# Kernel tuning notes

Measured on AMD Instinct MI355X. Metric: run time of the kernel, lower is better.

The kernel has to match this reference:

```python
import jax, jax.numpy as jnp
import numpy as np

B, IN_F, OUT_F, FAN_IN = 2048, 4096, 4096, 32


def setup_inputs() -> dict:
    key = jax.random.key(0)
    k1, k2, k3, k4 = jax.random.split(key, 4)
    x = jax.random.normal(k1, (B, IN_F), dtype=jnp.float32)
    weight = jax.random.normal(k2, (OUT_F, FAN_IN), dtype=jnp.float32) * (1.0 / np.sqrt(FAN_IN))
    bias = jax.random.normal(k3, (OUT_F,), dtype=jnp.float32) * 0.01
    indx_seqs = jnp.sort(jax.random.randint(k4, (OUT_F, FAN_IN), 0, IN_F, dtype=jnp.int64), axis=1)
    return {"x": x, "weight": weight, "bias": bias, "indx_seqs": indx_seqs}


def reference(x, weight, bias, indx_seqs):
    # gather: (B, OUT_F, FAN_IN) -- input[:, indx_seqs]
    gathered = jnp.take(x, indx_seqs, axis=1)
    # elementwise multiply by weight (OUT_F, FAN_IN), reduce over fan_in, add bias
    return jnp.sum(weight * gathered, axis=2) + bias
```

## Files before the change

kernel.cpp:

```cpp
#include <hip/hip_runtime.h>


constexpr int IN_F  = 4096;
constexpr int OUT_F = 4096;
constexpr int K     = 32;
constexpr int BT    = 8;
constexpr int THREADS = 512;
constexpr int ROWS_PER_BLOCK = 32;
constexpr int ITERS = ROWS_PER_BLOCK / BT;
constexpr int CPT = IN_F / THREADS;

typedef __fp16 h2_t __attribute__((ext_vector_type(2)));

__device__ __forceinline__ int pack_f16(float lo, float hi) {
    union { h2_t h; int i; } cv;
    cv.h = __builtin_amdgcn_cvt_pkrtz(lo, hi);
    return cv.i;
}
__device__ __forceinline__ float h_lo(int u) {
    union { int i; h2_t h; } cv; cv.i = u; return (float)cv.h[0];
}
__device__ __forceinline__ float h_hi(int u) {
    union { int i; h2_t h; } cv; cv.i = u; return (float)cv.h[1];
}

__global__ __launch_bounds__(THREADS)
void lc_kernel(const float* __restrict__ x,
               const float* __restrict__ w,
               const float* __restrict__ bias,
               const int* __restrict__ idx,
               float* __restrict__ out,
               int bchunks) {
    __shared__ int4 xs[IN_F];
    const int tid = threadIdx.x;
    const int ochunk = blockIdx.x / bchunks;
    const int bchunk = blockIdx.x % bchunks;
    const int o = ochunk * THREADS + tid;

    int   ao[K];
    float wr[K];
    const int4*   ip = reinterpret_cast<const int4*>(idx + (size_t)o * K);
    const float4* wp = reinterpret_cast<const float4*>(w + (size_t)o * K);
#pragma unroll
    for (int kk = 0; kk < K / 4; ++kk) {
        int4   i4 = ip[kk];
        float4 w4 = wp[kk];
        ao[4*kk+0] = i4.x << 4;  ao[4*kk+1] = i4.y << 4;
        ao[4*kk+2] = i4.z << 4;  ao[4*kk+3] = i4.w << 4;
        wr[4*kk+0] = w4.x;  wr[4*kk+1] = w4.y;
        wr[4*kk+2] = w4.z;  wr[4*kk+3] = w4.w;
    }
    const float bv = bias[o];
    const int b0 = bchunk * ROWS_PER_BLOCK;

    float pf[BT * CPT];

    {
        const float* xr = x + (size_t)b0 * IN_F;
#pragma unroll
        for (int j = 0; j < CPT; ++j)
#pragma unroll
            for (int r = 0; r < BT; ++r)
                pf[j * BT + r] = xr[(size_t)r * IN_F + tid + j * THREADS];
#pragma unroll
        for (int j = 0; j < CPT; ++j) {
            int4 pk;
            pk.x = pack_f16(pf[j*BT+0], pf[j*BT+1]);
            pk.y = pack_f16(pf[j*BT+2], pf[j*BT+3]);
            pk.z = pack_f16(pf[j*BT+4], pf[j*BT+5]);
            pk.w = pack_f16(pf[j*BT+6], pf[j*BT+7]);
            xs[tid + j * THREADS] = pk;
        }
    }
    __syncthreads();

    const char* xb = reinterpret_cast<const char*>(&xs[0]);

#pragma unroll
    for (int it = 0; it < ITERS; ++it) {
        if (it + 1 < ITERS) {
            const float* xr = x + (size_t)(b0 + (it + 1) * BT) * IN_F;
#pragma unroll
            for (int j = 0; j < CPT; ++j)
#pragma unroll
                for (int r = 0; r < BT; ++r)
                    pf[j * BT + r] = xr[(size_t)r * IN_F + tid + j * THREADS];
        }

        float acc[BT];
#pragma unroll
        for (int r = 0; r < BT; ++r) acc[r] = bv;
#pragma unroll
        for (int k = 0; k < K; ++k) {
            int4 v = *reinterpret_cast<const int4*>(xb + ao[k]);
            const float wk = wr[k];
            acc[0] += wk * h_lo(v.x);
            acc[1] += wk * h_hi(v.x);
            acc[2] += wk * h_lo(v.y);
            acc[3] += wk * h_hi(v.y);
            acc[4] += wk * h_lo(v.z);
            acc[5] += wk * h_hi(v.z);
            acc[6] += wk * h_lo(v.w);
            acc[7] += wk * h_hi(v.w);
        }

        float* op = out + (size_t)(b0 + it * BT) * OUT_F + o;
#pragma unroll
        for (int r = 0; r < BT; ++r) op[(size_t)r * OUT_F] = acc[r];

        if (it + 1 < ITERS) {
            __syncthreads();
#pragma unroll
            for (int j = 0; j < CPT; ++j) {
                int4 pk;
                pk.x = pack_f16(pf[j*BT+0], pf[j*BT+1]);
                pk.y = pack_f16(pf[j*BT+2], pf[j*BT+3]);
                pk.z = pack_f16(pf[j*BT+4], pf[j*BT+5]);
                pk.w = pack_f16(pf[j*BT+6], pf[j*BT+7]);
                xs[tid + j * THREADS] = pk;
            }
            __syncthreads();
        }
    }
}

extern "C" void kernel_launch(void* const* d_in, const int* in_sizes, int n_in,
                              void* d_out, int out_size, void* d_ws, size_t ws_size,
                              hipStream_t stream) {
    const float* x    = (const float*)d_in[0];
    const float* w    = (const float*)d_in[1];
    const float* bias = (const float*)d_in[2];
    const int*   idx  = (const int*)d_in[3];
    float* out = (float*)d_out;

    const int Bv = in_sizes[0] / IN_F;
    const int bchunks = Bv / ROWS_PER_BLOCK;
    const int ochunks = (in_sizes[1] / K) / THREADS;
    lc_kernel<<<dim3(ochunks * bchunks), dim3(THREADS), 0, stream>>>(
        x, w, bias, idx, out, bchunks);
}
```

Baseline: 41.30 us.

## Pre-pack x to fp16 in workspace and DMA tiles into LDS via global_load_lds

Adds a prep kernel that converts x into an fp16 interleaved layout (8 batch rows per 16-byte entry) in the workspace. The main kernel then loads each 64KB tile straight into LDS with global_load_lds and computes one 8-row group per block of 256 threads. This removes the per-block fp32 load, convert and LDS store path and the multi-iteration sync loop. The cost is an extra kernel launch, an extra write and read of the packed x buffer, and many more blocks that each reload idx and weights. The original kernel is kept as a fallback when the workspace is too small.

After: 67.60 us. 63.7% more time.

```diff
diff --git a/kernel.cpp b/kernel.cpp
--- a/kernel.cpp
+++ b/kernel.cpp
@@ -5,10 +5,8 @@
 constexpr int OUT_F = 4096;
 constexpr int K     = 32;
 constexpr int BT    = 8;
-constexpr int THREADS = 512;
-constexpr int ROWS_PER_BLOCK = 32;
-constexpr int ITERS = ROWS_PER_BLOCK / BT;
-constexpr int CPT = IN_F / THREADS;
+constexpr int MT    = 256;
+constexpr long long XT_BYTES = (long long)(2048 / BT) * IN_F * 16;
 
 typedef __fp16 h2_t __attribute__((ext_vector_type(2)));
 
@@ -24,18 +22,110 @@
     union { int i; h2_t h; } cv; cv.i = u; return (float)cv.h[1];
 }
 
-__global__ __launch_bounds__(THREADS)
-void lc_kernel(const float* __restrict__ x,
-               const float* __restrict__ w,
-               const float* __restrict__ bias,
-               const int* __restrict__ idx,
-               float* __restrict__ out,
-               int bchunks) {
+__global__ __launch_bounds__(256)
+void lc_prep(const float* __restrict__ x, int4* __restrict__ xT) {
+    const int bid  = blockIdx.x;
+    const int g    = bid >> 2;
+    const int part = bid & 3;
+    const int q    = part * 256 + threadIdx.x;
+    const float4* xr = reinterpret_cast<const float4*>(x + (size_t)g * BT * IN_F);
+    float4 r[BT];
+#pragma unroll
+    for (int i = 0; i < BT; ++i) r[i] = xr[(size_t)i * (IN_F / 4) + q];
+    int4* op = xT + (size_t)g * IN_F + 4 * q;
+#pragma unroll
+    for (int m = 0; m < 4; ++m) {
+        int4 pk;
+        pk.x = pack_f16(((const float*)&r[0])[m], ((const float*)&r[1])[m]);
+        pk.y = pack_f16(((const float*)&r[2])[m], ((const float*)&r[3])[m]);
+        pk.z = pack_f16(((const float*)&r[4])[m], ((const float*)&r[5])[m]);
+        pk.w = pack_f16(((const float*)&r[6])[m], ((const float*)&r[7])[m]);
+        op[m] = pk;
+    }
+}
+
+__global__ __launch_bounds__(MT)
+void lc_main(const int4* __restrict__ xT,
+             const float* __restrict__ w,
+             const float* __restrict__ bias,
+             const int* __restrict__ idx,
+             float* __restrict__ out,
+             int groups) {
+    __shared__ int4 xs[IN_F];
+    const int tid = threadIdx.x;
+    const int g   = blockIdx.x % groups;
+    const int oc  = blockIdx.x / groups;
+    const int o   = oc * MT + tid;
+
+    int   ao[K];
+    float wr[K];
+    const int4*   ip = reinterpret_cast<const int4*>(idx + (size_t)o * K);
+    const float4* wp = reinterpret_cast<const float4*>(w + (size_t)o * K);
+    int4   iq[K / 4];
+    float4 wq[K / 4];
+#pragma unroll
+    for (int kk = 0; kk < K / 4; ++kk) { iq[kk] = ip[kk]; wq[kk] = wp[kk]; }
+    const float bv = bias[o];
+
+    {
+        const char* gsrc = reinterpret_cast<const char*>(xT) + (size_t)g * (IN_F * 16);
+        char* lbase = reinterpret_cast<char*>(&xs[0]);
+        const int wbase = (tid & 192) << 4;
+        const int lane16 = tid << 4;
+#pragma unroll
+        for (int j = 0; j < 16; ++j) {
+            __builtin_amdgcn_global_load_lds(
+                (const __attribute__((address_space(1))) unsigned int*)(gsrc + j * 4096 + lane16),
+                (__attribute__((address_space(3))) unsigned int*)(lbase + j * 4096 + wbase),
+                16, 0, 0);
+        }
+    }
+    __syncthreads();
+
+#pragma unroll
+    for (int kk = 0; kk < K / 4; ++kk) {
+        ao[4*kk+0] = iq[kk].x << 4;  ao[4*kk+1] = iq[kk].y << 4;
+        ao[4*kk+2] = iq[kk].z << 4;  ao[4*kk+3] = iq[kk].w << 4;
+        wr[4*kk+0] = wq[kk].x;  wr[4*kk+1] = wq[kk].y;
+        wr[4*kk+2] = wq[kk].z;  wr[4*kk+3] = wq[kk].w;
+    }
+
+    const char* xb = reinterpret_cast<const char*>(&xs[0]);
+    float acc[BT];
+#pragma unroll
+    for (int r = 0; r < BT; ++r) acc[r] = bv;
+#pragma unroll
+    for (int k = 0; k < K; ++k) {
+        int4 v = *reinterpret_cast<const int4*>(xb + ao[k]);
+        const float wk = wr[k];
+        acc[0] += wk * h_lo(v.x);  acc[1] += wk * h_hi(v.x);
+        acc[2] += wk * h_lo(v.y);  acc[3] += wk * h_hi(v.y);
+        acc[4] += wk * h_lo(v.z);  acc[5] += wk * h_hi(v.z);
+        acc[6] += wk * h_lo(v.w);  acc[7] += wk * h_hi(v.w);
+    }
+
+    float* op = out + (size_t)(g * BT) * OUT_F + o;
+#pragma unroll
+    for (int r = 0; r < BT; ++r) op[(size_t)r * OUT_F] = acc[r];
+}
+
+constexpr int FB_THREADS = 512;
+constexpr int FB_RPB = 32;
+constexpr int FB_ITERS = FB_RPB / BT;
+constexpr int FB_CPT = IN_F / FB_THREADS;
+
+__global__ __launch_bounds__(FB_THREADS)
+void lc_fallback(const float* __restrict__ x,
+                 const float* __restrict__ w,
+                 const float* __restrict__ bias,
+                 const int* __restrict__ idx,
+                 float* __restrict__ out,
+                 int bchunks) {
     __shared__ int4 xs[IN_F];
     const int tid = threadIdx.x;
     const int ochunk = blockIdx.x / bchunks;
     const int bchunk = blockIdx.x % bchunks;
-    const int o = ochunk * THREADS + tid;
+    const int o = ochunk * FB_THREADS + tid;
 
     int   ao[K];
     float wr[K];
@@ -51,42 +141,39 @@
         wr[4*kk+2] = w4.z;  wr[4*kk+3] = w4.w;
     }
     const float bv = bias[o];
-    const int b0 = bchunk * ROWS_PER_BLOCK;
-
-    float pf[BT * CPT];
+    const int b0 = bchunk * FB_RPB;
+    float pf[BT * FB_CPT];
 
     {
         const float* xr = x + (size_t)b0 * IN_F;
 #pragma unroll
-        for (int j = 0; j < CPT; ++j)
+        for (int j = 0; j < FB_CPT; ++j)
 #pragma unroll
             for (int r = 0; r < BT; ++r)
-                pf[j * BT + r] = xr[(size_t)r * IN_F + tid + j * THREADS];
-#pragma unroll
-        for (int j = 0; j < CPT; ++j) {
+                pf[j * BT + r] = xr[(size_t)r * IN_F + tid + j * FB_THREADS];
+#pragma unroll
+        for (int j = 0; j < FB_CPT; ++j) {
             int4 pk;
             pk.x = pack_f16(pf[j*BT+0], pf[j*BT+1]);
             pk.y = pack_f16(pf[j*BT+2], pf[j*BT+3]);
             pk.z = pack_f16(pf[j*BT+4], pf[j*BT+5]);
             pk.w = pack_f16(pf[j*BT+6], pf[j*BT+7]);
-            xs[tid + j * THREADS] = pk;
+            xs[tid + j * FB_THREADS] = pk;
         }
     }
     __syncthreads();
-
     const char* xb = reinterpret_cast<const char*>(&xs[0]);
 
 #pragma unroll
-    for (int it = 0; it < ITERS; ++it) {
-        if (it + 1 < ITERS) {
+    for (int it = 0; it < FB_ITERS; ++it) {
+        if (it + 1 < FB_ITERS) {
             const float* xr = x + (size_t)(b0 + (it + 1) * BT) * IN_F;
 #pragma unroll
-            for (int j = 0; j < CPT; ++j)
+            for (int j = 0; j < FB_CPT; ++j)
 #pragma unroll
                 for (int r = 0; r < BT; ++r)
-                    pf[j * BT + r] = xr[(size_t)r * IN_F + tid + j * THREADS];
-        }
-
+                    pf[j * BT + r] = xr[(size_t)r * IN_F + tid + j * FB_THREADS];
+        }
         float acc[BT];
 #pragma unroll
         for (int r = 0; r < BT; ++r) acc[r] = bv;
@@ -94,30 +181,25 @@
         for (int k = 0; k < K; ++k) {
             int4 v = *reinterpret_cast<const int4*>(xb + ao[k]);
             const float wk = wr[k];
-            acc[0] += wk * h_lo(v.x);
-            acc[1] += wk * h_hi(v.x);
-            acc[2] += wk * h_lo(v.y);
-            acc[3] += wk * h_hi(v.y);
-            acc[4] += wk * h_lo(v.z);
-            acc[5] += wk * h_hi(v.z);
-            acc[6] += wk * h_lo(v.w);
-            acc[7] += wk * h_hi(v.w);
-        }
-
+            acc[0] += wk * h_lo(v.x);  acc[1] += wk * h_hi(v.x);
+            acc[2] += wk * h_lo(v.y);  acc[3] += wk * h_hi(v.y);
+            acc[4] += wk * h_lo(v.z);  acc[5] += wk * h_hi(v.z);
+            acc[6] += wk * h_lo(v.w);  acc[7] += wk * h_hi(v.w);
+        }
         float* op = out + (size_t)(b0 + it * BT) * OUT_F + o;
 #pragma unroll
         for (int r = 0; r < BT; ++r) op[(size_t)r * OUT_F] = acc[r];
 
-        if (it + 1 < ITERS) {
+        if (it + 1 < FB_ITERS) {
             __syncthreads();
 #pragma unroll
-            for (int j = 0; j < CPT; ++j) {
+            for (int j = 0; j < FB_CPT; ++j) {
                 int4 pk;
                 pk.x = pack_f16(pf[j*BT+0], pf[j*BT+1]);
                 pk.y = pack_f16(pf[j*BT+2], pf[j*BT+3]);
                 pk.z = pack_f16(pf[j*BT+4], pf[j*BT+5]);
                 pk.w = pack_f16(pf[j*BT+6], pf[j*BT+7]);
-                xs[tid + j * THREADS] = pk;
+                xs[tid + j * FB_THREADS] = pk;
             }
             __syncthreads();
         }
@@ -134,8 +216,18 @@
     float* out = (float*)d_out;
 
     const int Bv = in_sizes[0] / IN_F;
-    const int bchunks = Bv / ROWS_PER_BLOCK;
-    const int ochunks = (in_sizes[1] / K) / THREADS;
-    lc_kernel<<<dim3(ochunks * bchunks), dim3(THREADS), 0, stream>>>(
-        x, w, bias, idx, out, bchunks);
-}
+    const int groups = Bv / BT;
+
+    const long long xt_bytes = (long long)groups * IN_F * 16;
+    if ((long long)ws_size >= xt_bytes) {
+        int4* xT = (int4*)d_ws;
+        lc_prep<<<dim3(groups * 4), dim3(256), 0, stream>>>(x, xT);
+        const int ochunks = OUT_F / MT;
+        lc_main<<<dim3(ochunks * groups), dim3(MT), 0, stream>>>(
+            xT, w, bias, idx, out, groups);
+    } else {
+        const int bchunks = Bv / FB_RPB;
+        lc_fallback<<<dim3((OUT_F / FB_THREADS) * bchunks), dim3(FB_THREADS), 0, stream>>>(
+            x, w, bias, idx, out, bchunks);
+    }
+}
```
